# Performance work log

Measured on AMD Instinct MI355X. Metric: run time of the kernel, lower is better.

The kernel has to match this reference:

```python
import jax, jax.numpy as jnp
import numpy as np
import math

D_MODEL = 1024
NUM_HEADS = 16
HEAD_DIM = D_MODEL // NUM_HEADS  # 64
THETA = 10000.0
BATCH = 2
SEQ = 2048


def setup_inputs() -> dict:
    key = jax.random.key(0)
    ks = jax.random.split(key, 5)
    scale = 0.02
    return {
        "in_features": jax.random.normal(ks[0], (BATCH, SEQ, D_MODEL), jnp.float32),
        "q_proj": jax.random.normal(ks[1], (D_MODEL, D_MODEL), jnp.float32) * scale,
        "k_proj": jax.random.normal(ks[2], (D_MODEL, D_MODEL), jnp.float32) * scale,
        "v_proj": jax.random.normal(ks[3], (D_MODEL, D_MODEL), jnp.float32) * scale,
        "o_proj": jax.random.normal(ks[4], (D_MODEL, D_MODEL), jnp.float32) * scale,
        "token_positions": jnp.arange(SEQ, dtype=jnp.int32),
    }


def _rope(x, token_positions):
    # x: [b, h, s, head_dim]; interleaved even/odd rotation
    half = HEAD_DIM // 2
    inv_freq = 1.0 / (THETA ** (2.0 * jnp.arange(half, dtype=x.dtype) / HEAD_DIM))
    angle = token_positions.astype(x.dtype)[:, None] * inv_freq[None, :]  # [s, half]
    cos, sin = jnp.cos(angle), jnp.sin(angle)
    x_e, x_o = x[..., ::2], x[..., 1::2]
    r_e = x_e * cos - x_o * sin
    r_o = x_e * sin + x_o * cos
    # interleave back: [..., s, half, 2] -> [..., s, head_dim]
    return jnp.stack([r_e, r_o], axis=-1).reshape(x.shape)


def reference(in_features, q_proj, k_proj, v_proj, o_proj, token_positions):
    b, s, _ = in_features.shape
    # projections: weight layout is [d_out, d_in]
    Q = jnp.einsum('bsd,kd->bsk', in_features, q_proj)
    K = jnp.einsum('bsd,kd->bsk', in_features, k_proj)
    V = jnp.einsum('bsd,kd->bsk', in_features, v_proj)
    # split heads: [b, h, s, head_dim]
    Q = Q.reshape(b, s, NUM_HEADS, HEAD_DIM).transpose(0, 2, 1, 3)
    K = K.reshape(b, s, NUM_HEADS, HEAD_DIM).transpose(0, 2, 1, 3)
    V = V.reshape(b, s, NUM_HEADS, HEAD_DIM).transpose(0, 2, 1, 3)
    Q = _rope(Q, token_positions)
    K = _rope(K, token_positions)
    scores = jnp.einsum('bhnd,bhmd->bhnm', Q, K) / math.sqrt(HEAD_DIM)
    causal = jnp.tril(jnp.ones((s, s), dtype=bool))  # [s, s]
    scores = jnp.where(causal[None, None], scores, -jnp.inf)
    attn = jax.nn.softmax(scores, axis=-1)
    out = jnp.einsum('bhnm,bhmd->bhnd', attn, V)
    out = out.transpose(0, 2, 1, 3).reshape(b, s, D_MODEL)
    return jnp.einsum('bsv,dv->bsd', out, o_proj)
```

## Files before the change

kernel.cpp:

```cpp
#include <hip/hip_runtime.h>
#include <hip/hip_bf16.h>

#define D_MODEL 1024
#define NHEAD   16
#define HDIM    64
#define SEQQ    2048
#define NBATCH  2
#define MROWS   (NBATCH * SEQQ)

typedef unsigned short u16;
typedef __attribute__((ext_vector_type(8))) short short8;
typedef __attribute__((ext_vector_type(4))) short bf16x4;
typedef __attribute__((ext_vector_type(4))) float floatx4;

__device__ __forceinline__ u16 f2b(float f) {
    union { __hip_bfloat16 h; u16 u; } cv;
    cv.h = __float2bfloat16(f);
    return cv.u;
}
__device__ __forceinline__ float b2f(u16 u) {
    return __uint_as_float(((unsigned int)u) << 16);
}
__device__ __forceinline__ short8 load8(const u16* p) {
    return *reinterpret_cast<const short8*>(p);
}
__device__ __forceinline__ bf16x4 load4v(const u16* p) {
    return *reinterpret_cast<const bf16x4*>(p);
}
__device__ __forceinline__ unsigned pack2(float lo, float hi) {
    return ((unsigned)f2b(hi) << 16) | (unsigned)f2b(lo);
}
__device__ __forceinline__ void async_cp16(const void* g, void* l) {
    __builtin_amdgcn_global_load_lds(
        (const __attribute__((address_space(1))) void*)g,
        (__attribute__((address_space(3))) void*)l, 16, 0, 0);
}

__global__ void cvt_all(const float* __restrict__ X,
                        const float* __restrict__ w0, const float* __restrict__ w1,
                        const float* __restrict__ w2, const float* __restrict__ w3,
                        const int* __restrict__ pos,
                        u16* __restrict__ xo,
                        u16* __restrict__ o0, u16* __restrict__ o1,
                        u16* __restrict__ o2, u16* __restrict__ o3,
                        float2* __restrict__ tab) {
    const int z = blockIdx.y;
    const int i = blockIdx.x * 256 + threadIdx.x;
    if (z == 8) {
        if (i < SEQQ * 32) {
            const int j = i >> 11, s = i & (SEQQ - 1);
            const float p = (float)pos[s];
            const float inv = expf(-(float)j * (9.210340371976184f / 32.0f));
            float sn, cs;
            sincosf(p * inv, &sn, &cs);
            tab[i] = make_float2(cs, sn);
        }
        return;
    }
    const int n4 = (D_MODEL * D_MODEL) / 4;
    const float* in;
    u16* out;
    if (z < 4) { in = X + (size_t)z * n4 * 4;  out = xo + (size_t)z * n4 * 4; }
    else {
        in  = (z == 4) ? w0 : (z == 5) ? w1 : (z == 6) ? w2 : w3;
        out = (z == 4) ? o0 : (z == 5) ? o1 : (z == 6) ? o2 : o3;
    }
    int src = i;
    if (z == 4 || z == 5) {
        const int orow = i >> 8;
        const int g    = i & 255;
        const int irow = (orow & ~63) | (((orow & 31) << 1) | ((orow >> 5) & 1));
        src = irow * 256 + g;
    }
    float4 v = reinterpret_cast<const float4*>(in)[src];
    ushort4 o;
    o.x = f2b(v.x); o.y = f2b(v.y); o.z = f2b(v.z); o.w = f2b(v.w);
    reinterpret_cast<ushort4*>(out)[i] = o;
}

__global__ __launch_bounds__(256) void gemm_qkv(
    const u16* __restrict__ A,
    const u16* __restrict__ B0, const u16* __restrict__ B1, const u16* __restrict__ B2,
    u16* __restrict__ Qt, u16* __restrict__ Kt, u16* __restrict__ Vt,
    const float2* __restrict__ tab)
{
    const int K = D_MODEL;
    const int z = blockIdx.z;
    const u16* Bt = (z == 0) ? B0 : (z == 1 ? B1 : B2);

    __shared__ __attribute__((aligned(16))) u16 As[2][128 * 32];
    __shared__ __attribute__((aligned(16))) u16 Bs[2][128 * 32];

    const int tid  = threadIdx.x;
    const int w    = tid >> 6;
    const int lane = tid & 63;
    const int l15  = lane & 15;
    const int quad = lane >> 4;
    const int wm   = w >> 1, wn = w & 1;
    const int tm   = blockIdx.x * 128, tn = blockIdx.y * 128;

    floatx4 acc[4][4];
#pragma unroll
    for (int i = 0; i < 4; i++)
#pragma unroll
        for (int j = 0; j < 4; j++) {
            floatx4 zz = {0.f, 0.f, 0.f, 0.f};
            acc[i][j] = zz;
        }

    const int srow = lane >> 2;
    const int scol = (lane & 3) * 8;

    auto stage = [&](int buf, int k0) {
#pragma unroll
        for (int ch = w; ch < 8; ch += 4) {
            async_cp16(A  + (size_t)(tm + ch * 16 + srow) * K + k0 + scol, &As[buf][ch * 512]);
            async_cp16(Bt + (size_t)(tn + ch * 16 + srow) * K + k0 + scol, &Bs[buf][ch * 512]);
        }
    };

    stage(0, 0);

    for (int kt = 0; kt < 32; ++kt) {
        asm volatile("s_waitcnt vmcnt(0)" ::: "memory");
        __builtin_amdgcn_s_barrier();
        if (kt < 31) stage((kt + 1) & 1, (kt + 1) * 32);

        const u16* AsB = &As[kt & 1][0];
        const u16* BsB = &Bs[kt & 1][0];

        short8 af[4], bfr[4];
#pragma unroll
        for (int mi = 0; mi < 4; mi++)
            af[mi] = load8(&AsB[(wm * 64 + mi * 16 + l15) * 32 + quad * 8]);
#pragma unroll
        for (int ni = 0; ni < 4; ni++)
            bfr[ni] = load8(&BsB[(wn * 64 + ni * 16 + l15) * 32 + quad * 8]);
#pragma unroll
        for (int mi = 0; mi < 4; mi++)
#pragma unroll
            for (int ni = 0; ni < 4; ni++)
                acc[mi][ni] = __builtin_amdgcn_mfma_f32_16x16x32_bf16(af[mi], bfr[ni], acc[mi][ni], 0, 0, 0);
    }

    if (z == 2) {
#pragma unroll
        for (int mi = 0; mi < 4; mi++) {
            const int r0 = tm + wm * 64 + mi * 16 + quad * 4;
            const int bb = r0 >> 11, s0 = r0 & (SEQQ - 1);
#pragma unroll
            for (int ni = 0; ni < 4; ni++) {
                const int colb = tn + wn * 64 + ni * 16 + l15;
                const int d = colb & 63, hh = colb >> 6;
                ushort4 pk;
                pk.x = f2b(acc[mi][ni][0]);
                pk.y = f2b(acc[mi][ni][1]);
                pk.z = f2b(acc[mi][ni][2]);
                pk.w = f2b(acc[mi][ni][3]);
                *reinterpret_cast<ushort4*>(
                    &Vt[(((size_t)(bb * NHEAD + hh)) * HDIM + d) * SEQQ + s0]) = pk;
            }
        }
    } else {
        const float qsc = (z == 0) ? 0.18033688011112042f : 1.0f;
        u16* Outp = (z == 0) ? Qt : Kt;
        const int hh = (tn >> 6) + wn;
        float4 ta[2], tb[2];
        auto ldtab = [&](int g) {
            const int mi = g >> 1, ni = g & 1;
            const int qq = ni * 16 + l15;
            const int s0 = (tm + wm * 64 + mi * 16 + quad * 4) & (SEQQ - 1);
            ta[g & 1] = *reinterpret_cast<const float4*>(&tab[qq * SEQQ + s0]);
            tb[g & 1] = *reinterpret_cast<const float4*>(&tab[qq * SEQQ + s0 + 2]);
        };
        ldtab(0);
#pragma unroll
        for (int g = 0; g < 8; ++g) {
            if (g < 7) ldtab(g + 1);
            const int mi = g >> 1, ni = g & 1;
            const int qq = ni * 16 + l15;
            const int r0 = tm + wm * 64 + mi * 16 + quad * 4;
            const int bb = r0 >> 11, s0 = r0 & (SEQQ - 1);
            const float4 A4 = ta[g & 1], B4 = tb[g & 1];
            const float cs[4] = {A4.x, A4.z, B4.x, B4.z};
            const float sn[4] = {A4.y, A4.w, B4.y, B4.w};
#pragma unroll
            for (int rg = 0; rg < 4; rg++) {
                const float e = acc[mi][ni][rg];
                const float o = acc[mi][ni + 2][rg];
                const unsigned val =
                    (unsigned)f2b((e * cs[rg] - o * sn[rg]) * qsc) |
                    ((unsigned)f2b((e * sn[rg] + o * cs[rg]) * qsc) << 16);
                *reinterpret_cast<unsigned*>(
                    &Outp[(((size_t)(bb * NHEAD + hh)) * SEQQ + (s0 + rg)) * HDIM + 2 * qq]) = val;
            }
        }
    }
}

__global__ __launch_bounds__(256, 4) void attn_kernel(
    const u16* __restrict__ Qt, const u16* __restrict__ Kt, const u16* __restrict__ Vt,
    u16* __restrict__ Out)
{
    const int bid = blockIdx.x;
    const int xcd = bid & 7;
    const int u   = bid >> 3;
    const int col = xcd * 4 + (u & 3);
    const int m   = u >> 2;
    int qsub;
    if      (m < 8)  qsub = 31 - m;
    else if (m < 16) qsub = m - 8;
    else if (m < 24) qsub = 39 - m;
    else             qsub = m - 16;
    const int h = col & (NHEAD - 1), b = col >> 4;

    const int tid = threadIdx.x, w = tid >> 6, lane = tid & 63;
    const int l15 = lane & 15, quad = lane >> 4;
    const size_t bh = (size_t)(b * NHEAD + h);
    const u16* Qh = Qt + bh * SEQQ * HDIM;
    const u16* Kh = Kt + bh * SEQQ * HDIM;
    const u16* Vh = Vt + bh * HDIM * SEQQ;

    __shared__ __attribute__((aligned(16))) u16 Ks[2][64 * 64];
    __shared__ __attribute__((aligned(16))) u16 Vs[2][64 * 64];

    short8 ones;
#pragma unroll
    for (int i = 0; i < 8; i++) ones[i] = (short)0x3F80;

    const int rr  = lane >> 3;
    const int swz = ((lane & 7) ^ rr) * 8;
    auto stage = [&](int buf, int tt) {
        const int k0s = tt * 64;
        async_cp16(Kh + (size_t)(k0s + w * 8 + rr) * HDIM + swz,       &Ks[buf][w * 512]);
        async_cp16(Kh + (size_t)(k0s + (w + 4) * 8 + rr) * HDIM + swz, &Ks[buf][(w + 4) * 512]);
        async_cp16(Vh + (size_t)(w * 8 + rr) * SEQQ + k0s + swz,       &Vs[buf][w * 512]);
        async_cp16(Vh + (size_t)((w + 4) * 8 + rr) * SEQQ + k0s + swz, &Vs[buf][(w + 4) * 512]);
    };

    const int s7  = l15 & 7;
    const int sw1 = ((quad)     ^ s7) * 8;
    const int sw2 = ((quad + 4) ^ s7) * 8;
    const int vo0 = (((quad >> 1)    ) ^ s7) * 8 + (quad & 1) * 4;
    const int vo1 = (((quad >> 1) + 2) ^ s7) * 8 + (quad & 1) * 4;
    const int vo2 = (((quad >> 1) + 4) ^ s7) * 8 + (quad & 1) * 4;
    const int vo3 = (((quad >> 1) + 6) ^ s7) * 8 + (quad & 1) * 4;

    const int q0w   = qsub * 64 + w * 16;
    const int tmaxp = qsub;

    short8 qf[2];
#pragma unroll
    for (int kk = 0; kk < 2; kk++)
        qf[kk] = load8(&Qh[(size_t)(q0w + l15) * HDIM + kk * 32 + quad * 8]);

    floatx4 O[4];
    floatx4 l_acc = {0.f, 0.f, 0.f, 0.f};
#pragma unroll
    for (int c = 0; c < 4; c++) { floatx4 zz = {0.f, 0.f, 0.f, 0.f}; O[c] = zz; }

    stage(0, 0);

    for (int t = 0; t <= tmaxp; ++t) {
        asm volatile("s_waitcnt vmcnt(0)" ::: "memory");
        __builtin_amdgcn_s_barrier();
        if (t < tmaxp) stage((t + 1) & 1, t + 1);

        const u16* KsB = &Ks[t & 1][0];
        const u16* VsB = &Vs[t & 1][0];
        const int k0 = t * 64;

        floatx4 S[4];
        __builtin_amdgcn_s_setprio(1);
#pragma unroll
        for (int c = 0; c < 4; c++) {
            const int rowb = (c * 16 + l15) * 64;
            floatx4 zz = {0.f, 0.f, 0.f, 0.f};
            S[c] = __builtin_amdgcn_mfma_f32_16x16x32_bf16(load8(&KsB[rowb + sw1]), qf[0], zz,   0, 0, 0);
            S[c] = __builtin_amdgcn_mfma_f32_16x16x32_bf16(load8(&KsB[rowb + sw2]), qf[1], S[c], 0, 0, 0);
        }
        __builtin_amdgcn_s_setprio(0);

        if (t == tmaxp) {
            const int q = q0w + l15;
#pragma unroll
            for (int c = 0; c < 4; c++)
#pragma unroll
                for (int r = 0; r < 4; r++)
                    if (k0 + c * 16 + quad * 4 + r > q) S[c][r] = -1e30f;
        }

#pragma unroll
        for (int c = 0; c < 4; c++)
#pragma unroll
            for (int r = 0; r < 4; r++)
                S[c][r] = __builtin_amdgcn_exp2f(S[c][r]);

        union { short8 v; unsigned u[4]; } pf0, pf1;
        pf0.u[0] = pack2(S[0][0], S[0][1]);
        pf0.u[1] = pack2(S[0][2], S[0][3]);
        pf0.u[2] = pack2(S[1][0], S[1][1]);
        pf0.u[3] = pack2(S[1][2], S[1][3]);
        pf1.u[0] = pack2(S[2][0], S[2][1]);
        pf1.u[1] = pack2(S[2][2], S[2][3]);
        pf1.u[2] = pack2(S[3][0], S[3][1]);
        pf1.u[3] = pack2(S[3][2], S[3][3]);

        __builtin_amdgcn_s_setprio(1);
        l_acc = __builtin_amdgcn_mfma_f32_16x16x32_bf16(pf0.v, ones, l_acc, 0, 0, 0);
        l_acc = __builtin_amdgcn_mfma_f32_16x16x32_bf16(pf1.v, ones, l_acc, 0, 0, 0);

#pragma unroll
        for (int c2 = 0; c2 < 4; c2++) {
            const int rowb = (c2 * 16 + l15) * 64;
            bf16x4 a0 = load4v(&VsB[rowb + vo0]);
            bf16x4 a1 = load4v(&VsB[rowb + vo1]);
            bf16x4 a2 = load4v(&VsB[rowb + vo2]);
            bf16x4 a3 = load4v(&VsB[rowb + vo3]);
            short8 v0 = __builtin_shufflevector(a0, a1, 0, 1, 2, 3, 4, 5, 6, 7);
            short8 v1 = __builtin_shufflevector(a2, a3, 0, 1, 2, 3, 4, 5, 6, 7);
            O[c2] = __builtin_amdgcn_mfma_f32_16x16x32_bf16(pf0.v, v0, O[c2], 0, 0, 0);
            O[c2] = __builtin_amdgcn_mfma_f32_16x16x32_bf16(pf1.v, v1, O[c2], 0, 0, 0);
        }
        __builtin_amdgcn_s_setprio(0);
    }

    float inv_l[4];
#pragma unroll
    for (int r = 0; r < 4; r++) inv_l[r] = 1.0f / l_acc[r];

#pragma unroll
    for (int c2 = 0; c2 < 4; c2++)
#pragma unroll
        for (int r = 0; r < 4; r++) {
            const int q    = q0w + quad * 4 + r;
            const int colo = h * HDIM + c2 * 16 + l15;
            Out[(size_t)(b * SEQQ + q) * D_MODEL + colo] = f2b(O[c2][r] * inv_l[r]);
        }
}

__global__ __launch_bounds__(256) void gemm_o(
    const u16* __restrict__ A, const u16* __restrict__ Bt, float* __restrict__ C)
{
    const int K = D_MODEL, N = D_MODEL;
    __shared__ __attribute__((aligned(16))) u16 As[2][64 * 32];
    __shared__ __attribute__((aligned(16))) u16 Bs[2][128 * 32];

    const int tid  = threadIdx.x;
    const int w    = tid >> 6;
    const int lane = tid & 63;
    const int l15  = lane & 15;
    const int quad = lane >> 4;
    const int wm   = w >> 1, wn = w & 1;
    const int tm   = blockIdx.x * 64, tn = blockIdx.y * 128;

    floatx4 acc[2][4];
#pragma unroll
    for (int i = 0; i < 2; i++)
#pragma unroll
        for (int j = 0; j < 4; j++) {
            floatx4 z = {0.f, 0.f, 0.f, 0.f};
            acc[i][j] = z;
        }

    const int srow = lane >> 2;
    const int scol = (lane & 3) * 8;

    auto stage = [&](int buf, int k0) {
#pragma unroll
        for (int ch = w; ch < 12; ch += 4) {
            if (ch < 4) async_cp16(A  + (size_t)(tm + ch * 16 + srow) * K + k0 + scol, &As[buf][ch * 512]);
            else        async_cp16(Bt + (size_t)(tn + (ch - 4) * 16 + srow) * K + k0 + scol, &Bs[buf][(ch - 4) * 512]);
        }
    };

    stage(0, 0);

    for (int kt = 0; kt < 32; ++kt) {
        asm volatile("s_waitcnt vmcnt(0)" ::: "memory");
        __builtin_amdgcn_s_barrier();
        if (kt < 31) stage((kt + 1) & 1, (kt + 1) * 32);

        const u16* AsB = &As[kt & 1][0];
        const u16* BsB = &Bs[kt & 1][0];

        short8 af[2], bfr[4];
#pragma unroll
        for (int mi = 0; mi < 2; mi++)
            af[mi] = load8(&AsB[(wm * 32 + mi * 16 + l15) * 32 + quad * 8]);
#pragma unroll
        for (int ni = 0; ni < 4; ni++)
            bfr[ni] = load8(&BsB[(wn * 64 + ni * 16 + l15) * 32 + quad * 8]);
#pragma unroll
        for (int mi = 0; mi < 2; mi++)
#pragma unroll
            for (int ni = 0; ni < 4; ni++)
                acc[mi][ni] = __builtin_amdgcn_mfma_f32_16x16x32_bf16(af[mi], bfr[ni], acc[mi][ni], 0, 0, 0);
    }

#pragma unroll
    for (int mi = 0; mi < 2; mi++)
#pragma unroll
        for (int ni = 0; ni < 4; ni++)
#pragma unroll
            for (int rg = 0; rg < 4; rg++) {
                int row = tm + wm * 32 + mi * 16 + quad * 4 + rg;
                int col = tn + wn * 64 + ni * 16 + l15;
                C[(size_t)row * N + col] = acc[mi][ni][rg];
            }
}

extern "C" void kernel_launch(void* const* d_in, const int* in_sizes, int n_in,
                              void* d_out, int out_size, void* d_ws, size_t ws_size,
                              hipStream_t stream)
{
    const float* X  = (const float*)d_in[0];
    const float* Wq = (const float*)d_in[1];
    const float* Wk = (const float*)d_in[2];
    const float* Wv = (const float*)d_in[3];
    const float* Wo = (const float*)d_in[4];
    const int* tpos = (const int*)d_in[5];
    float* out = (float*)d_out;
    char* ws = (char*)d_ws;

    const size_t MB = (size_t)1 << 20;
    u16*    Xb  = (u16*)(ws + 0);
    u16*    WqB = (u16*)(ws + 8 * MB);
    u16*    WkB = (u16*)(ws + 10 * MB);
    u16*    WvB = (u16*)(ws + 12 * MB);
    u16*    WoB = (u16*)(ws + 14 * MB);
    float2* tab = (float2*)(ws + 16 * MB);
    u16*    Qt  = (u16*)(ws + 24 * MB);
    u16*    Kt  = (u16*)(ws + 32 * MB);
    u16*    Vt  = (u16*)(ws + 40 * MB);
    u16*   AOut = (u16*)(ws + 48 * MB);

    cvt_all<<<dim3(1024, 9), 256, 0, stream>>>(X, Wq, Wk, Wv, Wo, tpos,
                                               Xb, WqB, WkB, WvB, WoB, tab);

    gemm_qkv<<<dim3(32, 8, 3), 256, 0, stream>>>(Xb, WqB, WkB, WvB,
                                                 Qt, Kt, Vt, tab);
    attn_kernel<<<dim3(1024, 1, 1), 256, 0, stream>>>(Qt, Kt, Vt, AOut);
    gemm_o<<<dim3(64, 8), 256, 0, stream>>>(AOut, WoB, out);
}
```

Before: 184.4 us.

## Triple-buffer GEMM staging, swizzle LDS chunks, shrink O-proj tile

Both projection GEMMs move from double to triple buffering in LDS. The wait now uses a partial vmcnt so two stages of async copies stay in flight. The 16-byte chunk index within each 32-element row is XOR-swizzled on store and on load to cut LDS bank conflicts. The output projection switches to 64x64 tiles with twice as many blocks to raise occupancy. In exchange this uses more LDS, adds index arithmetic, and gives the O GEMM less reuse per tile.

```diff
diff --git a/kernel.cpp b/kernel.cpp
--- a/kernel.cpp
+++ b/kernel.cpp
@@ -88,8 +88,8 @@
     const int z = blockIdx.z;
     const u16* Bt = (z == 0) ? B0 : (z == 1 ? B1 : B2);
 
-    __shared__ __attribute__((aligned(16))) u16 As[2][128 * 32];
-    __shared__ __attribute__((aligned(16))) u16 Bs[2][128 * 32];
+    __shared__ __attribute__((aligned(16))) u16 As[3][128 * 32];
+    __shared__ __attribute__((aligned(16))) u16 Bs[3][128 * 32];
 
     const int tid  = threadIdx.x;
     const int w    = tid >> 6;
@@ -109,7 +109,7 @@
         }
 
     const int srow = lane >> 2;
-    const int scol = (lane & 3) * 8;
+    const int scol = (((lane & 3) ^ ((lane >> 4) & 3))) * 8;
 
     auto stage = [&](int buf, int k0) {
 #pragma unroll
@@ -120,22 +120,26 @@
     };
 
     stage(0, 0);
+    stage(1, 32);
+
+    const int rchunk = (quad ^ (l15 >> 2)) * 8;
 
     for (int kt = 0; kt < 32; ++kt) {
-        asm volatile("s_waitcnt vmcnt(0)" ::: "memory");
+        if (kt < 30) asm volatile("s_waitcnt vmcnt(4)" ::: "memory");
+        else         asm volatile("s_waitcnt vmcnt(0)" ::: "memory");
         __builtin_amdgcn_s_barrier();
-        if (kt < 31) stage((kt + 1) & 1, (kt + 1) * 32);
-
-        const u16* AsB = &As[kt & 1][0];
-        const u16* BsB = &Bs[kt & 1][0];
+        if (kt < 30) stage((kt + 2) % 3, (kt + 2) * 32);
+
+        const u16* AsB = &As[kt % 3][0];
+        const u16* BsB = &Bs[kt % 3][0];
 
         short8 af[4], bfr[4];
 #pragma unroll
         for (int mi = 0; mi < 4; mi++)
-            af[mi] = load8(&AsB[(wm * 64 + mi * 16 + l15) * 32 + quad * 8]);
+            af[mi] = load8(&AsB[(wm * 64 + mi * 16 + l15) * 32 + rchunk]);
 #pragma unroll
         for (int ni = 0; ni < 4; ni++)
-            bfr[ni] = load8(&BsB[(wn * 64 + ni * 16 + l15) * 32 + quad * 8]);
+            bfr[ni] = load8(&BsB[(wn * 64 + ni * 16 + l15) * 32 + rchunk]);
 #pragma unroll
         for (int mi = 0; mi < 4; mi++)
 #pragma unroll
@@ -343,8 +347,8 @@
     const u16* __restrict__ A, const u16* __restrict__ Bt, float* __restrict__ C)
 {
     const int K = D_MODEL, N = D_MODEL;
-    __shared__ __attribute__((aligned(16))) u16 As[2][64 * 32];
-    __shared__ __attribute__((aligned(16))) u16 Bs[2][128 * 32];
+    __shared__ __attribute__((aligned(16))) u16 As[3][64 * 32];
+    __shared__ __attribute__((aligned(16))) u16 Bs[3][64 * 32];
 
     const int tid  = threadIdx.x;
     const int w    = tid >> 6;
@@ -352,60 +356,61 @@
     const int l15  = lane & 15;
     const int quad = lane >> 4;
     const int wm   = w >> 1, wn = w & 1;
-    const int tm   = blockIdx.x * 64, tn = blockIdx.y * 128;
-
-    floatx4 acc[2][4];
+    const int tm   = blockIdx.x * 64, tn = blockIdx.y * 64;
+
+    floatx4 acc[2][2];
 #pragma unroll
     for (int i = 0; i < 2; i++)
 #pragma unroll
-        for (int j = 0; j < 4; j++) {
+        for (int j = 0; j < 2; j++) {
             floatx4 z = {0.f, 0.f, 0.f, 0.f};
             acc[i][j] = z;
         }
 
     const int srow = lane >> 2;
-    const int scol = (lane & 3) * 8;
+    const int scol = (((lane & 3) ^ ((lane >> 4) & 3))) * 8;
 
     auto stage = [&](int buf, int k0) {
-#pragma unroll
-        for (int ch = w; ch < 12; ch += 4) {
-            if (ch < 4) async_cp16(A  + (size_t)(tm + ch * 16 + srow) * K + k0 + scol, &As[buf][ch * 512]);
-            else        async_cp16(Bt + (size_t)(tn + (ch - 4) * 16 + srow) * K + k0 + scol, &Bs[buf][(ch - 4) * 512]);
-        }
+        async_cp16(A  + (size_t)(tm + w * 16 + srow) * K + k0 + scol, &As[buf][w * 512]);
+        async_cp16(Bt + (size_t)(tn + w * 16 + srow) * K + k0 + scol, &Bs[buf][w * 512]);
     };
 
     stage(0, 0);
+    stage(1, 32);
+
+    const int rchunk = (quad ^ (l15 >> 2)) * 8;
 
     for (int kt = 0; kt < 32; ++kt) {
-        asm volatile("s_waitcnt vmcnt(0)" ::: "memory");
+        if (kt < 30) asm volatile("s_waitcnt vmcnt(2)" ::: "memory");
+        else         asm volatile("s_waitcnt vmcnt(0)" ::: "memory");
         __builtin_amdgcn_s_barrier();
-        if (kt < 31) stage((kt + 1) & 1, (kt + 1) * 32);
-
-        const u16* AsB = &As[kt & 1][0];
-        const u16* BsB = &Bs[kt & 1][0];
-
-        short8 af[2], bfr[4];
+        if (kt < 30) stage((kt + 2) % 3, (kt + 2) * 32);
+
+        const u16* AsB = &As[kt % 3][0];
+        const u16* BsB = &Bs[kt % 3][0];
+
+        short8 af[2], bfr[2];
 #pragma unroll
         for (int mi = 0; mi < 2; mi++)
-            af[mi] = load8(&AsB[(wm * 32 + mi * 16 + l15) * 32 + quad * 8]);
-#pragma unroll
-        for (int ni = 0; ni < 4; ni++)
-            bfr[ni] = load8(&BsB[(wn * 64 + ni * 16 + l15) * 32 + quad * 8]);
+            af[mi] = load8(&AsB[(wm * 32 + mi * 16 + l15) * 32 + rchunk]);
+#pragma unroll
+        for (int ni = 0; ni < 2; ni++)
+            bfr[ni] = load8(&BsB[(wn * 32 + ni * 16 + l15) * 32 + rchunk]);
 #pragma unroll
         for (int mi = 0; mi < 2; mi++)
 #pragma unroll
-            for (int ni = 0; ni < 4; ni++)
+            for (int ni = 0; ni < 2; ni++)
                 acc[mi][ni] = __builtin_amdgcn_mfma_f32_16x16x32_bf16(af[mi], bfr[ni], acc[mi][ni], 0, 0, 0);
     }
 
 #pragma unroll
     for (int mi = 0; mi < 2; mi++)
 #pragma unroll
-        for (int ni = 0; ni < 4; ni++)
+        for (int ni = 0; ni < 2; ni++)
 #pragma unroll
             for (int rg = 0; rg < 4; rg++) {
                 int row = tm + wm * 32 + mi * 16 + quad * 4 + rg;
-                int col = tn + wn * 64 + ni * 16 + l15;
+                int col = tn + wn * 32 + ni * 16 + l15;
                 C[(size_t)row * N + col] = acc[mi][ni][rg];
             }
 }
@@ -441,5 +446,5 @@
     gemm_qkv<<<dim3(32, 8, 3), 256, 0, stream>>>(Xb, WqB, WkB, WvB,
                                                  Qt, Kt, Vt, tab);
     attn_kernel<<<dim3(1024, 1, 1), 256, 0, stream>>>(Qt, Kt, Vt, AOut);
-    gemm_o<<<dim3(64, 8), 256, 0, stream>>>(AOut, WoB, out);
-}
+    gemm_o<<<dim3(64, 16), 256, 0, stream>>>(AOut, WoB, out);
+}
```

New measurement: 187.7 us. About the same (+1.8%).
